# Kernel tuning notes

Hardware: AMD Instinct MI355X
Metric: run time of the kernel (lower is better)

## Reference

```python
import jax, jax.numpy as jnp
import numpy as np

# graph layout constants
B = 64        # number of graphs
NPG = 512     # nodes per graph
N = B * NPG   # total nodes
DEG = 16      # avg degree
E = N * DEG   # total edges
F_IN = 256
H, C = 4, 64  # heads, per-head dim
K = NPG // 2  # topk pooling keeps ratio=0.5 per graph


def setup_inputs() -> dict:
    key = jax.random.key(0)
    ks = jax.random.split(key, 8)
    x = jax.random.normal(ks[0], (N, F_IN), dtype=jnp.float32)
    # within-graph random edges (src -> dst), contiguous node ids per graph
    offs = jnp.repeat(jnp.arange(B, dtype=jnp.int64) * NPG, NPG * DEG)
    src = offs + jax.random.randint(ks[1], (E,), 0, NPG)
    dst = offs + jax.random.randint(ks[2], (E,), 0, NPG)
    edge_index = jnp.stack([src, dst]).astype(jnp.int64)
    W = jax.random.normal(ks[3], (F_IN, H, C), dtype=jnp.float32) / np.sqrt(F_IN)
    att_src = jax.random.normal(ks[4], (H, C), dtype=jnp.float32) / np.sqrt(C)
    att_dst = jax.random.normal(ks[5], (H, C), dtype=jnp.float32) / np.sqrt(C)
    bias = jnp.zeros((H * C,), dtype=jnp.float32)
    bn_gamma = jnp.ones((H * C,), dtype=jnp.float32)
    bn_beta = jnp.zeros((H * C,), dtype=jnp.float32)
    pool_weight = jax.random.normal(ks[6], (H * C,), dtype=jnp.float32) / np.sqrt(H * C)
    return {"x": x, "edge_index": edge_index, "W": W, "att_src": att_src,
            "att_dst": att_dst, "bias": bias, "bn_gamma": bn_gamma,
            "bn_beta": bn_beta, "pool_weight": pool_weight}


def reference(x, edge_index, W, att_src, att_dst, bias, bn_gamma, bn_beta, pool_weight):
    n = x.shape[0]
    # --- GATConv ---
    h = jnp.einsum('nf,fhc->nhc', x, W)                 # [N,H,C]
    a_src = jnp.sum(h * att_src, axis=-1)               # [N,H]
    a_dst = jnp.sum(h * att_dst, axis=-1)               # [N,H]
    loops = jnp.arange(n, dtype=edge_index.dtype)        # add_self_loops=True default
    src = jnp.concatenate([edge_index[0], loops])
    dst = jnp.concatenate([edge_index[1], loops])
    e = jax.nn.leaky_relu(a_src[src] + a_dst[dst], 0.2)  # [E+N,H]
    # scatter-softmax over edges grouped by destination node
    emax = jax.ops.segment_max(e, dst, num_segments=n)
    ex = jnp.exp(e - emax[dst])
    den = jax.ops.segment_sum(ex, dst, num_segments=n)
    alpha = ex / (den[dst] + 1e-16)                      # [E+N,H]
    msg = alpha[:, :, None] * h[src]                     # [E+N,H,C]
    out = jax.ops.segment_sum(msg, dst, num_segments=n)  # [N,H,C]
    feat = out.reshape(n, H * C) + bias                  # concat heads
    # --- ReLU + BatchNorm (batch stats, training mode) ---
    feat = jax.nn.relu(feat)
    mean = jnp.mean(feat, axis=0)
    var = jnp.var(feat, axis=0)
    feat = (feat - mean) * jax.lax.rsqrt(var + 1e-5) * bn_gamma + bn_beta
    # --- TopKPooling (score = x.w/||w||, keep top ratio per graph, gate by tanh) ---
    score = feat @ pool_weight / jnp.linalg.norm(pool_weight)  # [N]
    top_s, top_i = jax.lax.top_k(score.reshape(B, NPG), K)     # [B,K]
    fg = feat.reshape(B, NPG, H * C)
    sel = jnp.take_along_axis(fg, top_i[:, :, None], axis=1)    # [B,K,HC]
    pooled = sel * jnp.tanh(top_s)[:, :, None]
    return pooled.reshape(B * K, H * C)
```

## Files before the change

### kernel.cpp

```cpp
#include <hip/hip_runtime.h>
#include <math.h>

#define N_NODES 32768
#define NPG 512
#define NGRAPH 64
#define KKEEP 256
#define CAP 64

typedef __attribute__((ext_vector_type(8))) short short8;
typedef __attribute__((ext_vector_type(4))) float f32x4;

__device__ __forceinline__ unsigned short f2bf(float v) {
  unsigned u = __builtin_bit_cast(unsigned, v);
  u = (u + 0x7FFFu + ((u >> 16) & 1u)) >> 16;
  return (unsigned short)u;
}
__device__ __forceinline__ float bf2f(unsigned short u) {
  unsigned v = ((unsigned)u) << 16;
  return __builtin_bit_cast(float, v);
}

__global__ __launch_bounds__(256) void k_hist_conv(
    const int* __restrict__ ei, int E, int* __restrict__ cnt,
    unsigned short* __restrict__ nbr,
    const float* __restrict__ W,
    unsigned short* __restrict__ wth, unsigned short* __restrict__ wtl,
    unsigned short* __restrict__ wtll) {
  const int t = threadIdx.x;
  if (blockIdx.x < 2048) {
    int e = blockIdx.x * 256 + t;
    if (e < E) {
      int s = ei[e];
      int d = ei[E + e];
      int slot = atomicAdd(&cnt[d], 1);
      if (slot < CAP) nbr[(size_t)d * CAP + slot] = (unsigned short)(s & (NPG - 1));
    }
  } else {
    int bw = blockIdx.x - 2048;
    int n = bw * 4 + (t >> 6);
    int k = (t & 63) * 4;
    unsigned short hb[4], lb[4], qb[4];
#pragma unroll
    for (int j = 0; j < 4; j++) {
      float v = W[(size_t)(k + j) * 256 + n];
      unsigned short hh = f2bf(v);
      float e1 = v - bf2f(hh);
      unsigned short ll = f2bf(e1);
      float e2 = e1 - bf2f(ll);
      hb[j] = hh; lb[j] = ll; qb[j] = f2bf(e2);
    }
    *(uint2*)&wth[(size_t)n * 256 + k] = *(uint2*)&hb[0];
    *(uint2*)&wtl[(size_t)n * 256 + k] = *(uint2*)&lb[0];
    *(uint2*)&wtll[(size_t)n * 256 + k] = *(uint2*)&qb[0];
  }
}

__global__ __launch_bounds__(256) void k_gemm(
    const float* __restrict__ x,
    const unsigned short* __restrict__ wth, const unsigned short* __restrict__ wtl,
    const unsigned short* __restrict__ wtll,
    const float* __restrict__ attS, const float* __restrict__ attD,
    float* __restrict__ h, float* __restrict__ a_src, float* __restrict__ a_dst) {
  __shared__ unsigned short lds[24576];
  const int t = threadIdx.x;
  const int bid = blockIdx.x;
  const int mb = (bid & 7) * 32 + (bid >> 4);
  const int nh = (bid >> 3) & 1;
  const int row0 = mb * 128;
  const int wid = t >> 6, lane = t & 63;
  const int q = lane >> 4, ln = lane & 15;
  const int wm = (wid >> 1) * 64, wn = (wid & 1) * 64;
  f32x4 acc[4][4] = {};

  for (int kc = 0; kc < 8; kc++) {
    const int k0 = kc * 32;
#pragma unroll
    for (int i = 0; i < 2; i++) {
      int c = i * 256 + t;
      int r = c >> 2, cq = c & 3;
      size_t ga = (size_t)(row0 + r) * 256 + k0 + cq * 8;
      float4 f0 = *(const float4*)&x[ga];
      float4 f1 = *(const float4*)&x[ga + 4];
      float ff[8] = {f0.x, f0.y, f0.z, f0.w, f1.x, f1.y, f1.z, f1.w};
      unsigned short hs[8], ls[8], qs[8];
#pragma unroll
      for (int j = 0; j < 8; j++) {
        unsigned short hh = f2bf(ff[j]);
        float e1 = ff[j] - bf2f(hh);
        unsigned short ll = f2bf(e1);
        float e2 = e1 - bf2f(ll);
        hs[j] = hh; ls[j] = ll; qs[j] = f2bf(e2);
      }
      *(uint4*)&lds[((0 * 4 + cq) * 128 + r) * 8] = *(uint4*)&hs[0];
      *(uint4*)&lds[((1 * 4 + cq) * 128 + r) * 8] = *(uint4*)&ls[0];
      *(uint4*)&lds[((2 * 4 + cq) * 128 + r) * 8] = *(uint4*)&qs[0];
      size_t gb = (size_t)(nh * 128 + r) * 256 + k0 + cq * 8;
      *(uint4*)&lds[12288 + ((0 * 4 + cq) * 128 + r) * 8] = *(const uint4*)&wth[gb];
      *(uint4*)&lds[12288 + ((1 * 4 + cq) * 128 + r) * 8] = *(const uint4*)&wtl[gb];
      *(uint4*)&lds[12288 + ((2 * 4 + cq) * 128 + r) * 8] = *(const uint4*)&wtll[gb];
    }
    __syncthreads();
    short8 ah[4], al[4], aq[4];
#pragma unroll
    for (int mt = 0; mt < 4; mt++) {
      int r = wm + mt * 16 + ln;
      ah[mt] = *(const short8*)&lds[((0 * 4 + q) * 128 + r) * 8];
      al[mt] = *(const short8*)&lds[((1 * 4 + q) * 128 + r) * 8];
      aq[mt] = *(const short8*)&lds[((2 * 4 + q) * 128 + r) * 8];
    }
#pragma unroll
    for (int nt = 0; nt < 4; nt++) {
      int r = wn + nt * 16 + ln;
      short8 bh = *(const short8*)&lds[12288 + ((0 * 4 + q) * 128 + r) * 8];
      short8 bl = *(const short8*)&lds[12288 + ((1 * 4 + q) * 128 + r) * 8];
      short8 bq = *(const short8*)&lds[12288 + ((2 * 4 + q) * 128 + r) * 8];
#pragma unroll
      for (int mt = 0; mt < 4; mt++) {
        acc[mt][nt] = __builtin_amdgcn_mfma_f32_16x16x32_bf16(ah[mt], bh, acc[mt][nt], 0, 0, 0);
        acc[mt][nt] = __builtin_amdgcn_mfma_f32_16x16x32_bf16(ah[mt], bl, acc[mt][nt], 0, 0, 0);
        acc[mt][nt] = __builtin_amdgcn_mfma_f32_16x16x32_bf16(al[mt], bh, acc[mt][nt], 0, 0, 0);
        acc[mt][nt] = __builtin_amdgcn_mfma_f32_16x16x32_bf16(ah[mt], bq, acc[mt][nt], 0, 0, 0);
        acc[mt][nt] = __builtin_amdgcn_mfma_f32_16x16x32_bf16(al[mt], bl, acc[mt][nt], 0, 0, 0);
        acc[mt][nt] = __builtin_amdgcn_mfma_f32_16x16x32_bf16(aq[mt], bh, acc[mt][nt], 0, 0, 0);
      }
    }
    __syncthreads();
  }
  const int head = nh * 2 + (wid & 1);
  float sA[4], sD[4];
#pragma unroll
  for (int nt = 0; nt < 4; nt++) {
    int n = nh * 128 + wn + nt * 16 + ln;
    sA[nt] = attS[n];
    sD[nt] = attD[n];
  }
  float2* epi = (float2*)lds;
#pragma unroll
  for (int mt = 0; mt < 4; mt++) {
#pragma unroll
    for (int reg = 0; reg < 4; reg++) {
      int m = row0 + wm + mt * 16 + q * 4 + reg;
      float ps = 0.f, pd = 0.f;
#pragma unroll
      for (int nt = 0; nt < 4; nt++) {
        float v = acc[mt][nt][reg];
        h[(size_t)m * 256 + nh * 128 + wn + nt * 16 + ln] = v;
        ps = fmaf(v, sA[nt], ps);
        pd = fmaf(v, sD[nt], pd);
      }
      epi[(((wid * 4 + q) * 16) + mt * 4 + reg) * 18 + ln] = make_float2(ps, pd);
    }
  }
  __syncthreads();
  {
    const int q2 = lane >> 4, rr = lane & 15;
    const int base = (((wid * 4 + q2) * 16) + rr) * 18;
    float ps = 0.f, pd = 0.f;
#pragma unroll
    for (int i = 0; i < 16; i++) {
      float2 v = epi[base + i];
      ps += v.x;
      pd += v.y;
    }
    int m = row0 + wm + (rr >> 2) * 16 + q2 * 4 + (rr & 3);
    a_src[m * 4 + head] = ps;
    a_dst[m * 4 + head] = pd;
  }
}

__global__ __launch_bounds__(256) void k_agg(
    const float* __restrict__ h, const float* __restrict__ a_src,
    const float* __restrict__ a_dst, const int* __restrict__ cnt,
    const unsigned short* __restrict__ nbr, const float* __restrict__ bias,
    float* __restrict__ feat) {
  __shared__ float p_lds[4][68][4];
  __shared__ int s_lds[4][68];
  const int wv = threadIdx.x >> 6;
  const int lane = threadIdx.x & 63;
  int nb = (blockIdx.x & 7) * (N_NODES / 4 / 8) + (blockIdx.x >> 3);
  const int node = nb * 4 + wv;
  const int head = lane >> 4;
  const int li = lane & 15;
  const int c0 = lane * 4;
  const int base = node & ~(NPG - 1);
  const float ad = a_dst[node * 4 + head];
  int n = cnt[node];
  if (n > CAP) n = CAP;
  float e_reg[5];
  int srcs[5];
  int nit = 0;
  float m = -1e30f;
  for (int j = li; j <= n; j += 16) {
    int s = (j < n) ? base + (int)nbr[(size_t)node * CAP + j] : node;
    float e = a_src[s * 4 + head] + ad;
    e = (e > 0.f) ? e : 0.2f * e;
    srcs[nit] = s;
    e_reg[nit++] = e;
    m = fmaxf(m, e);
  }
#pragma unroll
  for (int d = 1; d < 16; d <<= 1) m = fmaxf(m, __shfl_xor(m, d, 16));
  float l = 0.f;
  for (int i = 0; i < nit; i++) {
    int j = li + i * 16;
    float p = __expf(e_reg[i] - m);
    l += p;
    p_lds[wv][j][head] = p;
    if (head == 0) s_lds[wv][j] = srcs[i];
  }
#pragma unroll
  for (int d = 1; d < 16; d <<= 1) l += __shfl_xor(l, d, 16);
  const float linv = 1.f / (l + 1e-16f);
  __builtin_amdgcn_s_waitcnt(0);
  float4 acc0 = make_float4(0.f, 0.f, 0.f, 0.f);
  float4 acc1 = make_float4(0.f, 0.f, 0.f, 0.f);
  int j = 0;
  for (; j + 1 <= n; j += 2) {
    float p0 = p_lds[wv][j][head];
    float p1 = p_lds[wv][j + 1][head];
    int s0 = s_lds[wv][j];
    int s1 = s_lds[wv][j + 1];
    float4 h0 = *(const float4*)&h[(size_t)s0 * 256 + c0];
    float4 h1 = *(const float4*)&h[(size_t)s1 * 256 + c0];
    acc0.x = fmaf(p0, h0.x, acc0.x); acc1.x = fmaf(p1, h1.x, acc1.x);
    acc0.y = fmaf(p0, h0.y, acc0.y); acc1.y = fmaf(p1, h1.y, acc1.y);
    acc0.z = fmaf(p0, h0.z, acc0.z); acc1.z = fmaf(p1, h1.z, acc1.z);
    acc0.w = fmaf(p0, h0.w, acc0.w); acc1.w = fmaf(p1, h1.w, acc1.w);
  }
  if (j <= n) {
    float p0 = p_lds[wv][j][head];
    int s0 = s_lds[wv][j];
    float4 h0 = *(const float4*)&h[(size_t)s0 * 256 + c0];
    acc0.x = fmaf(p0, h0.x, acc0.x);
    acc0.y = fmaf(p0, h0.y, acc0.y);
    acc0.z = fmaf(p0, h0.z, acc0.z);
    acc0.w = fmaf(p0, h0.w, acc0.w);
  }
  const float4 b4 = *(const float4*)&bias[c0];
  float4 o;
  o.x = fmaxf(fmaf(acc0.x + acc1.x, linv, b4.x), 0.f);
  o.y = fmaxf(fmaf(acc0.y + acc1.y, linv, b4.y), 0.f);
  o.z = fmaxf(fmaf(acc0.z + acc1.z, linv, b4.z), 0.f);
  o.w = fmaxf(fmaf(acc0.w + acc1.w, linv, b4.w), 0.f);
  *(float4*)&feat[(size_t)node * 256 + c0] = o;
}

__global__ __launch_bounds__(256) void k_bn_partial(const float* __restrict__ feat,
                                                    double* __restrict__ psum,
                                                    double* __restrict__ psq) {
  const int c = threadIdx.x;
  const int r0 = blockIdx.x * 128;
  double s = 0.0, q = 0.0;
  for (int i = 0; i < 128; i++) {
    double v = (double)feat[(size_t)(r0 + i) * 256 + c];
    s += v;
    q += v * v;
  }
  psum[blockIdx.x * 256 + c] = s;
  psq[blockIdx.x * 256 + c] = q;
}

__global__ __launch_bounds__(1024) void k_bn_final(
    const double* __restrict__ psum, const double* __restrict__ psq,
    const float* __restrict__ gam, const float* __restrict__ bet,
    const float* __restrict__ pw, float* __restrict__ cA, float* __restrict__ cB,
    float* __restrict__ sv) {
  __shared__ double reds[4][256];
  __shared__ double redq[4][256];
  __shared__ double wsq[256];
  __shared__ double sb[256];
  const int t = threadIdx.x;
  const int c = t & 255, sl = t >> 8;
  double s = 0.0, q = 0.0;
  for (int i = sl * 64; i < sl * 64 + 64; i++) {
    s += psum[i * 256 + c];
    q += psq[i * 256 + c];
  }
  reds[sl][c] = s;
  redq[sl][c] = q;
  if (sl == 0) {
    double w = (double)pw[c];
    wsq[c] = w * w;
  }
  __syncthreads();
  if (t == 0) {
    double nn = 0.0;
    for (int i = 0; i < 256; i++) nn += wsq[i];
    wsq[0] = sqrt(nn);
  }
  __syncthreads();
  if (sl == 0) {
    s = reds[0][c] + reds[1][c] + reds[2][c] + reds[3][c];
    q = redq[0][c] + redq[1][c] + redq[2][c] + redq[3][c];
    double mean = s / (double)N_NODES;
    double var = q / (double)N_NODES - mean * mean;
    double a = (double)gam[c] / sqrt(var + 1e-5);
    double cb = (double)bet[c] - mean * a;
    cA[c] = (float)a;
    cB[c] = (float)cb;
    double pwnv = (double)pw[c] / wsq[0];
    sv[c] = (float)(a * pwnv);
    sb[c] = cb * pwnv;
  }
  __syncthreads();
  if (t == 0) {
    double s0 = 0.0;
    for (int i = 0; i < 256; i++) s0 += sb[i];
    sv[256] = (float)s0;
  }
}

__global__ __launch_bounds__(256) void k_score(
    const float* __restrict__ feat, const float* __restrict__ sv,
    float* __restrict__ score) {
  const int lane = threadIdx.x & 63;
  const int node = blockIdx.x * 4 + (threadIdx.x >> 6);
  const int c0 = lane * 4;
  float4 f = *(const float4*)&feat[(size_t)node * 256 + c0];
  float4 w = *(const float4*)&sv[c0];
  float p = f.x * w.x + f.y * w.y + f.z * w.z + f.w * w.w;
#pragma unroll
  for (int d = 1; d < 64; d <<= 1) p += __shfl_xor(p, d, 64);
  if (lane == 0) score[node] = p + sv[256];
}

__global__ __launch_bounds__(256) void k_topk(
    const float* __restrict__ score, const float* __restrict__ feat,
    const float* __restrict__ cA, const float* __restrict__ cB,
    float* __restrict__ out) {
  __shared__ float ss[NPG];
  __shared__ int rnk[64];
  __shared__ float gt[64];
  const int g = blockIdx.x >> 3;
  const int part = blockIdx.x & 7;
  const int t = threadIdx.x;
  ss[t] = score[g * NPG + t];
  ss[t + 256] = score[g * NPG + t + 256];
  __syncthreads();
  const int ln = t & 3;
  const int ndl = part * 64 + (t >> 2);
  const float s = ss[ndl];
  int rank = 0;
  for (int j = ln * 128; j < ln * 128 + 128; j++) {
    float sj = ss[j];
    rank += (sj > s || (sj == s && j < ndl)) ? 1 : 0;
  }
  rank += __shfl_xor(rank, 1);
  rank += __shfl_xor(rank, 2);
  if (ln == 0) {
    rnk[t >> 2] = rank;
    gt[t >> 2] = tanhf(s);
  }
  __syncthreads();
  for (int idx = t; idx < 64 * 64; idx += 256) {
    int r = idx >> 6;
    int rank2 = rnk[r];
    if (rank2 < KKEEP) {
      int c4 = (idx & 63) * 4;
      int node = g * NPG + part * 64 + r;
      float4 f = *(const float4*)&feat[(size_t)node * 256 + c4];
      float4 a = *(const float4*)&cA[c4];
      float4 b = *(const float4*)&cB[c4];
      float tg = gt[r];
      float4 o;
      o.x = fmaf(f.x, a.x, b.x) * tg;
      o.y = fmaf(f.y, a.y, b.y) * tg;
      o.z = fmaf(f.z, a.z, b.z) * tg;
      o.w = fmaf(f.w, a.w, b.w) * tg;
      *(float4*)&out[(size_t)(g * KKEEP + rank2) * 256 + c4] = o;
    }
  }
}

extern "C" void kernel_launch(void* const* d_in, const int* in_sizes, int n_in,
                              void* d_out, int out_size, void* d_ws, size_t ws_size,
                              hipStream_t stream) {
  const float* x    = (const float*)d_in[0];
  const int*   ei   = (const int*)d_in[1];
  const float* W    = (const float*)d_in[2];
  const float* attS = (const float*)d_in[3];
  const float* attD = (const float*)d_in[4];
  const float* bias = (const float*)d_in[5];
  const float* gam  = (const float*)d_in[6];
  const float* bet  = (const float*)d_in[7];
  const float* pw   = (const float*)d_in[8];
  float* out = (float*)d_out;
  const int E = in_sizes[1] / 2;

  char* p = (char*)d_ws;
  float* h     = (float*)p; p += (size_t)N_NODES * 256 * 4;
  float* feat  = (float*)p; p += (size_t)N_NODES * 256 * 4;
  float* a_src = (float*)p; p += (size_t)N_NODES * 4 * 4;
  float* a_dst = (float*)p; p += (size_t)N_NODES * 4 * 4;
  float* score = (float*)p; p += (size_t)N_NODES * 4;
  double* psum = (double*)p; p += (size_t)256 * 256 * 8;
  double* psq  = (double*)p; p += (size_t)256 * 256 * 8;
  float* cA    = (float*)p; p += 256 * 4;
  float* cB    = (float*)p; p += 256 * 4;
  float* sv    = (float*)p; p += 260 * 4;
  unsigned short* wth  = (unsigned short*)p; p += (size_t)256 * 256 * 2;
  unsigned short* wtl  = (unsigned short*)p; p += (size_t)256 * 256 * 2;
  unsigned short* wtll = (unsigned short*)p; p += (size_t)256 * 256 * 2;
  int* cnt     = (int*)p;   p += (size_t)N_NODES * 4;
  unsigned short* nbr = (unsigned short*)p; p += (size_t)N_NODES * CAP * 2;

  hipMemsetAsync(cnt, 0, (size_t)N_NODES * 4, stream);
  k_hist_conv<<<2112, 256, 0, stream>>>(ei, E, cnt, nbr, W, wth, wtl, wtll);
  k_gemm<<<512, 256, 0, stream>>>(x, wth, wtl, wtll, attS, attD, h, a_src, a_dst);
  k_agg<<<N_NODES / 4, 256, 0, stream>>>(h, a_src, a_dst, cnt, nbr, bias, feat);
  k_bn_partial<<<256, 256, 0, stream>>>(feat, psum, psq);
  k_bn_final<<<1, 1024, 0, stream>>>(psum, psq, gam, bet, pw, cA, cB, sv);
  k_score<<<N_NODES / 4, 256, 0, stream>>>(feat, sv, score);
  k_topk<<<NGRAPH * 8, 256, 0, stream>>>(score, feat, cA, cB, out);
}
```

Measured before the change: 214.4 us.

## Build per-graph neighbor lists in LDS and fuse BN partial/final via ticket

The edge histogram now runs one block per graph and counts destinations with shared-memory atomics. Because each block writes all of its graph's counts, the cnt memset is no longer needed. The two BatchNorm kernels become a single kernel: each block writes partial sums, and the last block to arrive (found with an atomic ticket) does the final reduction. This removes one memset and one kernel launch and moves the histogram atomics off global memory, but the histogram phase now has only 64 blocks and so less parallelism, and each block serially processes 8192 edges.

```diff
diff --git a/kernel.cpp b/kernel.cpp
--- a/kernel.cpp
+++ b/kernel.cpp
@@ -20,24 +20,34 @@
   return __builtin_bit_cast(float, v);
 }
 
-__global__ __launch_bounds__(256) void k_hist_conv(
+__global__ __launch_bounds__(512) void k_histW(
     const int* __restrict__ ei, int E, int* __restrict__ cnt,
     unsigned short* __restrict__ nbr,
     const float* __restrict__ W,
     unsigned short* __restrict__ wth, unsigned short* __restrict__ wtl,
-    unsigned short* __restrict__ wtll) {
+    unsigned short* __restrict__ wtll, int* __restrict__ ticket) {
   const int t = threadIdx.x;
-  if (blockIdx.x < 2048) {
-    int e = blockIdx.x * 256 + t;
-    if (e < E) {
-      int s = ei[e];
-      int d = ei[E + e];
-      int slot = atomicAdd(&cnt[d], 1);
-      if (slot < CAP) nbr[(size_t)d * CAP + slot] = (unsigned short)(s & (NPG - 1));
-    }
+  if (blockIdx.x < 64) {
+    __shared__ int lcnt[NPG];
+    const int g = blockIdx.x;
+    lcnt[t] = 0;
+    if (g == 0 && t == 0) *ticket = 0;
+    __syncthreads();
+    const int e0 = g * (NPG * 16);
+#pragma unroll 4
+    for (int i = 0; i < 16; i++) {
+      int e = e0 + i * 512 + t;
+      if (e < E) {
+        int s = ei[e];
+        int dl = ei[E + e] & (NPG - 1);
+        int slot = atomicAdd(&lcnt[dl], 1);
+        if (slot < CAP) nbr[(size_t)(g * NPG + dl) * CAP + slot] = (unsigned short)(s & (NPG - 1));
+      }
+    }
+    __syncthreads();
+    cnt[g * NPG + t] = lcnt[t];
   } else {
-    int bw = blockIdx.x - 2048;
-    int n = bw * 4 + (t >> 6);
+    int n = (blockIdx.x - 64) * 8 + (t >> 6);
     int k = (t & 63) * 4;
     unsigned short hb[4], lb[4], qb[4];
 #pragma unroll
@@ -245,32 +255,35 @@
   *(float4*)&feat[(size_t)node * 256 + c0] = o;
 }
 
-__global__ __launch_bounds__(256) void k_bn_partial(const float* __restrict__ feat,
-                                                    double* __restrict__ psum,
-                                                    double* __restrict__ psq) {
-  const int c = threadIdx.x;
-  const int r0 = blockIdx.x * 128;
-  double s = 0.0, q = 0.0;
-  for (int i = 0; i < 128; i++) {
-    double v = (double)feat[(size_t)(r0 + i) * 256 + c];
-    s += v;
-    q += v * v;
-  }
-  psum[blockIdx.x * 256 + c] = s;
-  psq[blockIdx.x * 256 + c] = q;
-}
-
-__global__ __launch_bounds__(1024) void k_bn_final(
-    const double* __restrict__ psum, const double* __restrict__ psq,
+__global__ __launch_bounds__(1024) void k_bn(
+    const float* __restrict__ feat,
+    double* __restrict__ psum, double* __restrict__ psq,
     const float* __restrict__ gam, const float* __restrict__ bet,
     const float* __restrict__ pw, float* __restrict__ cA, float* __restrict__ cB,
-    float* __restrict__ sv) {
+    float* __restrict__ sv, int* __restrict__ ticket) {
+  const int t = threadIdx.x;
+  const int c = t & 255, sl = t >> 8;
+  {
+    const int r0 = blockIdx.x * 512 + sl * 128;
+    double s = 0.0, q = 0.0;
+    for (int i = 0; i < 128; i++) {
+      double v = (double)feat[(size_t)(r0 + i) * 256 + c];
+      s += v;
+      q += v * v;
+    }
+    psum[(blockIdx.x * 4 + sl) * 256 + c] = s;
+    psq[(blockIdx.x * 4 + sl) * 256 + c] = q;
+  }
+  __threadfence();
+  __syncthreads();
+  __shared__ int isLast;
+  if (t == 0) isLast = (atomicAdd(ticket, 1) == 63) ? 1 : 0;
+  __syncthreads();
+  if (!isLast) return;
   __shared__ double reds[4][256];
   __shared__ double redq[4][256];
   __shared__ double wsq[256];
   __shared__ double sb[256];
-  const int t = threadIdx.x;
-  const int c = t & 255, sl = t >> 8;
   double s = 0.0, q = 0.0;
   for (int i = sl * 64; i < sl * 64 + 64; i++) {
     s += psum[i * 256 + c];
@@ -403,13 +416,12 @@
   unsigned short* wtll = (unsigned short*)p; p += (size_t)256 * 256 * 2;
   int* cnt     = (int*)p;   p += (size_t)N_NODES * 4;
   unsigned short* nbr = (unsigned short*)p; p += (size_t)N_NODES * CAP * 2;
-
-  hipMemsetAsync(cnt, 0, (size_t)N_NODES * 4, stream);
-  k_hist_conv<<<2112, 256, 0, stream>>>(ei, E, cnt, nbr, W, wth, wtl, wtll);
+  int* ticket  = (int*)p;   p += 4;
+
+  k_histW<<<96, 512, 0, stream>>>(ei, E, cnt, nbr, W, wth, wtl, wtll, ticket);
   k_gemm<<<512, 256, 0, stream>>>(x, wth, wtl, wtll, attS, attD, h, a_src, a_dst);
   k_agg<<<N_NODES / 4, 256, 0, stream>>>(h, a_src, a_dst, cnt, nbr, bias, feat);
-  k_bn_partial<<<256, 256, 0, stream>>>(feat, psum, psq);
-  k_bn_final<<<1, 1024, 0, stream>>>(psum, psq, gam, bet, pw, cA, cB, sv);
+  k_bn<<<64, 1024, 0, stream>>>(feat, psum, psq, gam, bet, pw, cA, cB, sv, ticket);
   k_score<<<N_NODES / 4, 256, 0, stream>>>(feat, sv, score);
   k_topk<<<NGRAPH * 8, 256, 0, stream>>>(score, feat, cA, cB, out);
 }
```

Result: slower. 227.7 us (+6.2%).
